# Kernel tuning notes

Hardware: AMD Instinct MI355X
Metric: run time of the kernel (lower is better)

The kernel has to match this reference:

```python
import jax, jax.numpy as jnp
import numpy as np

NUM_BOND_TYPE = 6
NUM_BOND_DIRECTION = 3
N_NODES = 20000
N_EDGES = 320000
HIDDEN = 256
OUT = 256
N_MASK = 2000


def setup_inputs() -> dict:
    key = jax.random.key(0)
    ks = jax.random.split(key, 12)
    x = jax.random.normal(ks[0], (N_NODES, HIDDEN), dtype=jnp.float32)
    edge_index = jax.random.randint(ks[1], (2, N_EDGES), 0, N_NODES, dtype=jnp.int64)
    edge_attr = jax.random.randint(ks[2], (N_EDGES, 2), 0, 3, dtype=jnp.int64)
    mask_node_indices = jax.random.randint(ks[3], (N_MASK,), 0, N_NODES, dtype=jnp.int64)
    # parameters (torch Linear convention: y = x @ W.T + b)
    def xavier(k, shape):
        fan_in, fan_out = shape[1], shape[0]
        lim = float(np.sqrt(6.0 / (fan_in + fan_out)))
        return jax.random.uniform(k, shape, jnp.float32, -lim, lim)
    prelu_a = jnp.asarray(0.25, dtype=jnp.float32)  # torch PReLU default
    W_enc = xavier(ks[4], (HIDDEN, HIDDEN))          # enc_to_dec, no bias
    E1 = xavier(ks[5], (NUM_BOND_TYPE, HIDDEN))
    E2 = xavier(ks[6], (NUM_BOND_DIRECTION, HIDDEN))
    W1 = xavier(ks[7], (2 * HIDDEN, HIDDEN))
    b1 = jnp.zeros((2 * HIDDEN,), jnp.float32)
    W2 = xavier(ks[8], (OUT, 2 * HIDDEN))
    b2 = jnp.zeros((OUT,), jnp.float32)
    return {"x": x, "edge_index": edge_index, "edge_attr": edge_attr,
            "mask_node_indices": mask_node_indices, "prelu_a": prelu_a,
            "W_enc": W_enc, "E1": E1, "E2": E2,
            "W1": W1, "b1": b1, "W2": W2, "b2": b2}


def reference(x, edge_index, edge_attr, mask_node_indices, prelu_a,
              W_enc, E1, E2, W1, b1, W2, b2):
    N = x.shape[0]
    # PReLU -> enc_to_dec linear (no bias) -> zero masked rows
    x = jnp.where(x >= 0, x, prelu_a * x)
    x = x @ W_enc.T
    x = x.at[mask_node_indices].set(0.0)
    # add self loops: (i,i) edges with attr (4, 0)
    loop = jnp.arange(N, dtype=edge_index.dtype)
    ei = jnp.concatenate([edge_index, jnp.stack([loop, loop])], axis=1)  # [2, E+N]
    loop_attr = jnp.concatenate(
        [jnp.full((N, 1), 4, edge_attr.dtype), jnp.zeros((N, 1), edge_attr.dtype)], axis=1)
    ea = jnp.concatenate([edge_attr, loop_attr], axis=0)                 # [E+N, 2]
    edge_emb = E1[ea[:, 0]] + E2[ea[:, 1]]                               # [E+N, D]
    src, dst = ei[0], ei[1]                                              # j -> i
    msg = x[src] + edge_emb                                              # [E+N, D]
    aggr = jax.ops.segment_sum(msg, dst, num_segments=N)                 # [N, D]
    # GIN MLP: Linear -> ReLU -> Linear
    h = jax.nn.relu(aggr @ W1.T + b1)
    return h @ W2.T + b2
```

## Files before the change

### kernel.cpp

```cpp
#include <hip/hip_runtime.h>

#define HIDDEN 256
#define CAP 64

typedef _Float16 h4_t __attribute__((ext_vector_type(4)));
typedef _Float16 h8_t __attribute__((ext_vector_type(8)));
typedef float    f4_t __attribute__((ext_vector_type(4)));

typedef const __attribute__((address_space(1))) void* gbl_ptr_t;
typedef __attribute__((address_space(3))) void*       lds_ptr_t;

__global__ __launch_bounds__(256) void k_prep(
        const float* __restrict__ x, _Float16* __restrict__ xh,
        const float* __restrict__ prelu_a, int M, int Mpad, int nb_x,
        const int* __restrict__ ei, const int* __restrict__ ea, int E,
        int* __restrict__ cnt, int* __restrict__ csr, int nb_fill,
        const float* __restrict__ W_enc, const float* __restrict__ W1,
        const float* __restrict__ W2, _Float16* __restrict__ Whenc,
        _Float16* __restrict__ Wh1, _Float16* __restrict__ Wh2, int nb_w,
        const int* __restrict__ mask, unsigned char* __restrict__ flags, int NM) {
    int b = blockIdx.x;
    int t = threadIdx.x;
    if (b < nb_x) {
        int base = (b * 256 + t) * 4;
        if (base >= Mpad * HIDDEN) return;
        int row = base >> 8;
        h4_t o;
        if (row < M) {
            float pa = *prelu_a;
            f4_t v = *(const f4_t*)(x + base);
            o.x = (_Float16)(v.x >= 0.f ? v.x : pa * v.x);
            o.y = (_Float16)(v.y >= 0.f ? v.y : pa * v.y);
            o.z = (_Float16)(v.z >= 0.f ? v.z : pa * v.z);
            o.w = (_Float16)(v.w >= 0.f ? v.w : pa * v.w);
        } else {
            o = (h4_t)(_Float16)0.f;
        }
        *(h4_t*)(xh + base) = o;
        return;
    }
    b -= nb_x;
    if (b < nb_fill) {
        int e = b * 256 + t;
        if (e >= E) return;
        int src = ei[e];
        int dst = ei[E + e];
        int combo = ea[2 * e] * 3 + ea[2 * e + 1];
        int slot = atomicAdd(&cnt[dst], 1);
        csr[dst * CAP + slot] = src | (combo << 16);
        return;
    }
    b -= nb_fill;
    if (b < nb_w) {
        const int n0 = HIDDEN * HIDDEN, n1 = 2 * HIDDEN * HIDDEN, n2 = HIDDEN * 2 * HIDDEN;
        int base = (b * 256 + t) * 4;
        const float* s; _Float16* d; int off;
        if (base < n0) { s = W_enc; d = Whenc; off = base; }
        else if (base < n0 + n1) { s = W1; d = Wh1; off = base - n0; }
        else if (base < n0 + n1 + n2) { s = W2; d = Wh2; off = base - n0 - n1; }
        else return;
        f4_t v = *(const f4_t*)(s + off);
        h4_t o; o.x = (_Float16)v.x; o.y = (_Float16)v.y;
        o.z = (_Float16)v.z; o.w = (_Float16)v.w;
        *(h4_t*)(d + off) = o;
        return;
    }
    b -= nb_w;
    {
        int i = b * 256 + t;
        if (i < NM) flags[mask[i]] = 1;
    }
}

__global__ __launch_bounds__(256) void k_aggregate(
        const _Float16* __restrict__ xe,
        const float* __restrict__ E1, const float* __restrict__ E2,
        const int* __restrict__ cnt, const int* __restrict__ csr,
        _Float16* __restrict__ aggr, int N, int Mpad) {
    __shared__ float e12[18 * HIDDEN];
    int t = threadIdx.x;
    for (int idx = t; idx < 18 * HIDDEN; idx += 256) {
        int combo = idx >> 8, c = idx & 255;
        int a1 = combo / 3, a2 = combo - a1 * 3;
        e12[idx] = E1[a1 * HIDDEN + c] + E2[a2 * HIDDEN + c];
    }
    __syncthreads();
    int node = blockIdx.x * 4 + (t >> 6);
    if (node >= Mpad) return;
    int lane = t & 63;
    int c0 = lane * 4;
    if (node >= N) {
        *(h4_t*)(aggr + (size_t)node * HIDDEN + c0) = (h4_t)(_Float16)0.f;
        return;
    }

    h4_t hs = *(const h4_t*)(xe + (size_t)node * HIDDEN + c0);
    const f4_t se = *(const f4_t*)&e12[12 * HIDDEN + c0];
    f4_t acc;
    acc.x = (float)hs.x + se.x; acc.y = (float)hs.y + se.y;
    acc.z = (float)hs.z + se.z; acc.w = (float)hs.w + se.w;

    const int* lst = csr + (size_t)node * CAP;
    int deg = cnt[node];
    int e = 0;
    for (; e + 1 < deg; e += 2) {
        int p0 = lst[e], p1 = lst[e + 1];
        h4_t h0 = *(const h4_t*)(xe + (size_t)(p0 & 0xFFFF) * HIDDEN + c0);
        h4_t h1 = *(const h4_t*)(xe + (size_t)(p1 & 0xFFFF) * HIDDEN + c0);
        f4_t e0 = *(const f4_t*)&e12[(p0 >> 16) * HIDDEN + c0];
        f4_t e1 = *(const f4_t*)&e12[(p1 >> 16) * HIDDEN + c0];
        acc.x += (float)h0.x + e0.x + (float)h1.x + e1.x;
        acc.y += (float)h0.y + e0.y + (float)h1.y + e1.y;
        acc.z += (float)h0.z + e0.z + (float)h1.z + e1.z;
        acc.w += (float)h0.w + e0.w + (float)h1.w + e1.w;
    }
    if (e < deg) {
        int p0 = lst[e];
        h4_t h0 = *(const h4_t*)(xe + (size_t)(p0 & 0xFFFF) * HIDDEN + c0);
        f4_t e0 = *(const f4_t*)&e12[(p0 >> 16) * HIDDEN + c0];
        acc.x += (float)h0.x + e0.x; acc.y += (float)h0.y + e0.y;
        acc.z += (float)h0.z + e0.z; acc.w += (float)h0.w + e0.w;
    }
    h4_t o;
    o.x = (_Float16)acc.x; o.y = (_Float16)acc.y;
    o.z = (_Float16)acc.z; o.w = (_Float16)acc.w;
    *(h4_t*)(aggr + (size_t)node * HIDDEN + c0) = o;
}

template <bool RELU, bool HAS_BIAS, bool OUT_F16, bool MASK>
__global__ __launch_bounds__(256) void k_mfma_gemm(
        const _Float16* __restrict__ A, const _Float16* __restrict__ B,
        const float* __restrict__ bias, void* __restrict__ Cout,
        const unsigned char* __restrict__ flags,
        int Mstore, int N, int K) {
    __shared__ _Float16 As[128 * 32];
    __shared__ _Float16 Bs[128 * 32];
    int t = threadIdx.x;
    int w = t >> 6, L = t & 63;
    int m0 = blockIdx.x * 128, n0 = blockIdx.y * 128;
    int wm = (w >> 1) * 64, wn = (w & 1) * 64;
    int lrow = L & 15, lk = (L >> 4) * 8;

    f4_t acc[4][4] = {};

    int c0 = t, c1 = t + 256;
    int r0 = c0 >> 2, o0 = (c0 & 3) * 8;
    int r1 = c1 >> 2, o1 = (c1 & 3) * 8;

    for (int k0 = 0; k0 < K; k0 += 32) {
        __builtin_amdgcn_global_load_lds((gbl_ptr_t)(A + (size_t)(m0 + r0) * K + k0 + o0),
                                         (lds_ptr_t)(As + c0 * 8), 16, 0, 0);
        __builtin_amdgcn_global_load_lds((gbl_ptr_t)(A + (size_t)(m0 + r1) * K + k0 + o1),
                                         (lds_ptr_t)(As + c1 * 8), 16, 0, 0);
        __builtin_amdgcn_global_load_lds((gbl_ptr_t)(B + (size_t)(n0 + r0) * K + k0 + o0),
                                         (lds_ptr_t)(Bs + c0 * 8), 16, 0, 0);
        __builtin_amdgcn_global_load_lds((gbl_ptr_t)(B + (size_t)(n0 + r1) * K + k0 + o1),
                                         (lds_ptr_t)(Bs + c1 * 8), 16, 0, 0);
        __syncthreads();

        h8_t af[4], bf[4];
#pragma unroll
        for (int i = 0; i < 4; ++i)
            af[i] = *(const h8_t*)&As[(wm + i * 16 + lrow) * 32 + lk];
#pragma unroll
        for (int j = 0; j < 4; ++j)
            bf[j] = *(const h8_t*)&Bs[(wn + j * 16 + lrow) * 32 + lk];
#pragma unroll
        for (int i = 0; i < 4; ++i)
#pragma unroll
            for (int j = 0; j < 4; ++j)
                acc[i][j] = __builtin_amdgcn_mfma_f32_16x16x32_f16(af[i], bf[j], acc[i][j], 0, 0, 0);
        __syncthreads();
    }

    int lcol = L & 15, lr4 = (L >> 4) * 4;
    float zmul[4][4];
#pragma unroll
    for (int i = 0; i < 4; ++i)
#pragma unroll
        for (int r = 0; r < 4; ++r) {
            int row = m0 + wm + i * 16 + lr4 + r;
            zmul[i][r] = (MASK && flags[row]) ? 0.f : 1.f;
        }
#pragma unroll
    for (int j = 0; j < 4; ++j) {
        int col = n0 + wn + j * 16 + lcol;
        float bv = HAS_BIAS ? bias[col] : 0.f;
#pragma unroll
        for (int i = 0; i < 4; ++i) {
#pragma unroll
            for (int r = 0; r < 4; ++r) {
                int row = m0 + wm + i * 16 + lr4 + r;
                float v = (acc[i][j][r] + bv) * zmul[i][r];
                if (RELU) v = v > 0.f ? v : 0.f;
                if (OUT_F16) {
                    ((_Float16*)Cout)[(size_t)row * N + col] = (_Float16)v;
                } else {
                    if (row < Mstore) ((float*)Cout)[(size_t)row * N + col] = v;
                }
            }
        }
    }
}

extern "C" void kernel_launch(void* const* d_in, const int* in_sizes, int n_in,
                              void* d_out, int out_size, void* d_ws, size_t ws_size,
                              hipStream_t stream) {
    const float* x       = (const float*)d_in[0];
    const int*   ei      = (const int*)d_in[1];
    const int*   ea      = (const int*)d_in[2];
    const int*   mask    = (const int*)d_in[3];
    const float* prelu_a = (const float*)d_in[4];
    const float* W_enc   = (const float*)d_in[5];
    const float* E1      = (const float*)d_in[6];
    const float* E2      = (const float*)d_in[7];
    const float* W1      = (const float*)d_in[8];
    const float* b1      = (const float*)d_in[9];
    const float* W2      = (const float*)d_in[10];
    const float* b2      = (const float*)d_in[11];
    float*       out     = (float*)d_out;

    int N  = in_sizes[0] / HIDDEN;
    int E  = in_sizes[1] / 2;
    int NM = in_sizes[3];
    int Mpad = ((N + 127) / 128) * 128;

    char* ws = (char*)d_ws;
    size_t off = 0;
    _Float16* xh    = (_Float16*)(ws + off); off += (size_t)Mpad * HIDDEN * 2;
    _Float16* XEh   = (_Float16*)(ws + off); off += (size_t)Mpad * HIDDEN * 2;
    _Float16* AGh   = (_Float16*)(ws + off); off += (size_t)Mpad * HIDDEN * 2;
    _Float16* Hh    = (_Float16*)(ws + off); off += (size_t)Mpad * 2 * HIDDEN * 2;
    _Float16* Whenc = (_Float16*)(ws + off); off += (size_t)HIDDEN * HIDDEN * 2;
    _Float16* Wh1   = (_Float16*)(ws + off); off += (size_t)2 * HIDDEN * HIDDEN * 2;
    _Float16* Wh2   = (_Float16*)(ws + off); off += (size_t)HIDDEN * 2 * HIDDEN * 2;
    int* cnt        = (int*)(ws + off);      off += (size_t)N * 4;
    unsigned char* flags = (unsigned char*)(ws + off); off += (size_t)Mpad;
    off = (off + 15) & ~(size_t)15;
    int* csr        = (int*)(ws + off);      off += (size_t)N * CAP * 4;

    hipMemsetAsync(cnt, 0, (size_t)N * 4 + (size_t)Mpad, stream);

    int nb_x    = (Mpad * HIDDEN / 4 + 255) / 256;
    int nb_fill = (E + 255) / 256;
    int wtot4   = (HIDDEN * HIDDEN + 2 * HIDDEN * HIDDEN + HIDDEN * 2 * HIDDEN) / 4;
    int nb_w    = (wtot4 + 255) / 256;
    int nb_m    = (NM + 255) / 256;
    k_prep<<<nb_x + nb_fill + nb_w + nb_m, 256, 0, stream>>>(
        x, xh, prelu_a, N, Mpad, nb_x,
        ei, ea, E, cnt, csr, nb_fill,
        W_enc, W1, W2, Whenc, Wh1, Wh2, nb_w,
        mask, flags, NM);

    dim3 g1(Mpad / 128, HIDDEN / 128);
    k_mfma_gemm<false, false, true, true><<<g1, 256, 0, stream>>>(
        xh, Whenc, nullptr, XEh, flags, N, HIDDEN, HIDDEN);

    k_aggregate<<<(Mpad + 3) / 4, 256, 0, stream>>>(XEh, E1, E2, cnt, csr, AGh, N, Mpad);

    dim3 g2(Mpad / 128, 2 * HIDDEN / 128);
    k_mfma_gemm<true, true, true, false><<<g2, 256, 0, stream>>>(
        AGh, Wh1, b1, Hh, nullptr, N, 2 * HIDDEN, HIDDEN);

    dim3 g3(Mpad / 128, HIDDEN / 128);
    k_mfma_gemm<false, true, false, false><<<g3, 256, 0, stream>>>(
        Hh, Wh2, b2, out, nullptr, N, HIDDEN, 2 * HIDDEN);
}
```

Baseline: 188.7 us.

## Double-buffer GEMM tiles, shrink to 128x64 blocks, and use fp16 adds in aggregation

The GEMM kernel now uses 2-wave 128-thread blocks with 128x64 output tiles and double-buffered LDS staging, so the next K slice loads while MFMAs run and one barrier per step is removed. The aggregation kernel stores the edge-embedding table as fp16, unrolls the neighbour loop by four, and sums pairs of messages in fp16 before accumulating in fp32. This aims to cut load latency stalls and LDS traffic, at the cost of some precision in the fp16 partial sums and a changed GEMM occupancy and tiling.

```diff
diff --git a/kernel.cpp b/kernel.cpp
--- a/kernel.cpp
+++ b/kernel.cpp
@@ -77,49 +77,60 @@
         const float* __restrict__ E1, const float* __restrict__ E2,
         const int* __restrict__ cnt, const int* __restrict__ csr,
         _Float16* __restrict__ aggr, int N, int Mpad) {
-    __shared__ float e12[18 * HIDDEN];
+    __shared__ __align__(16) _Float16 e12h[18 * HIDDEN];
     int t = threadIdx.x;
-    for (int idx = t; idx < 18 * HIDDEN; idx += 256) {
-        int combo = idx >> 8, c = idx & 255;
+    for (int idx = t; idx < 18 * 64; idx += 256) {
+        int combo = idx >> 6, c4 = (idx & 63) * 4;
         int a1 = combo / 3, a2 = combo - a1 * 3;
-        e12[idx] = E1[a1 * HIDDEN + c] + E2[a2 * HIDDEN + c];
+        f4_t v1 = *(const f4_t*)(E1 + a1 * HIDDEN + c4);
+        f4_t v2 = *(const f4_t*)(E2 + a2 * HIDDEN + c4);
+        h4_t o;
+        o.x = (_Float16)(v1.x + v2.x); o.y = (_Float16)(v1.y + v2.y);
+        o.z = (_Float16)(v1.z + v2.z); o.w = (_Float16)(v1.w + v2.w);
+        *(h4_t*)(e12h + combo * HIDDEN + c4) = o;
     }
     __syncthreads();
     int node = blockIdx.x * 4 + (t >> 6);
     if (node >= Mpad) return;
-    int lane = t & 63;
-    int c0 = lane * 4;
+    int c0 = (t & 63) * 4;
     if (node >= N) {
         *(h4_t*)(aggr + (size_t)node * HIDDEN + c0) = (h4_t)(_Float16)0.f;
         return;
     }
 
     h4_t hs = *(const h4_t*)(xe + (size_t)node * HIDDEN + c0);
-    const f4_t se = *(const f4_t*)&e12[12 * HIDDEN + c0];
+    h4_t se = *(const h4_t*)(e12h + 12 * HIDDEN + c0);
     f4_t acc;
-    acc.x = (float)hs.x + se.x; acc.y = (float)hs.y + se.y;
-    acc.z = (float)hs.z + se.z; acc.w = (float)hs.w + se.w;
+    acc.x = (float)hs.x + (float)se.x; acc.y = (float)hs.y + (float)se.y;
+    acc.z = (float)hs.z + (float)se.z; acc.w = (float)hs.w + (float)se.w;
 
     const int* lst = csr + (size_t)node * CAP;
     int deg = cnt[node];
     int e = 0;
-    for (; e + 1 < deg; e += 2) {
-        int p0 = lst[e], p1 = lst[e + 1];
+    for (; e + 3 < deg; e += 4) {
+        int p0 = lst[e], p1 = lst[e + 1], p2 = lst[e + 2], p3 = lst[e + 3];
         h4_t h0 = *(const h4_t*)(xe + (size_t)(p0 & 0xFFFF) * HIDDEN + c0);
         h4_t h1 = *(const h4_t*)(xe + (size_t)(p1 & 0xFFFF) * HIDDEN + c0);
-        f4_t e0 = *(const f4_t*)&e12[(p0 >> 16) * HIDDEN + c0];
-        f4_t e1 = *(const f4_t*)&e12[(p1 >> 16) * HIDDEN + c0];
-        acc.x += (float)h0.x + e0.x + (float)h1.x + e1.x;
-        acc.y += (float)h0.y + e0.y + (float)h1.y + e1.y;
-        acc.z += (float)h0.z + e0.z + (float)h1.z + e1.z;
-        acc.w += (float)h0.w + e0.w + (float)h1.w + e1.w;
-    }
-    if (e < deg) {
+        h4_t h2 = *(const h4_t*)(xe + (size_t)(p2 & 0xFFFF) * HIDDEN + c0);
+        h4_t h3 = *(const h4_t*)(xe + (size_t)(p3 & 0xFFFF) * HIDDEN + c0);
+        h4_t q0 = *(const h4_t*)(e12h + (p0 >> 16) * HIDDEN + c0);
+        h4_t q1 = *(const h4_t*)(e12h + (p1 >> 16) * HIDDEN + c0);
+        h4_t q2 = *(const h4_t*)(e12h + (p2 >> 16) * HIDDEN + c0);
+        h4_t q3 = *(const h4_t*)(e12h + (p3 >> 16) * HIDDEN + c0);
+        h4_t s01 = (h0 + q0) + (h1 + q1);
+        h4_t s23 = (h2 + q2) + (h3 + q3);
+        acc.x += (float)s01.x + (float)s23.x;
+        acc.y += (float)s01.y + (float)s23.y;
+        acc.z += (float)s01.z + (float)s23.z;
+        acc.w += (float)s01.w + (float)s23.w;
+    }
+    for (; e < deg; ++e) {
         int p0 = lst[e];
         h4_t h0 = *(const h4_t*)(xe + (size_t)(p0 & 0xFFFF) * HIDDEN + c0);
-        f4_t e0 = *(const f4_t*)&e12[(p0 >> 16) * HIDDEN + c0];
-        acc.x += (float)h0.x + e0.x; acc.y += (float)h0.y + e0.y;
-        acc.z += (float)h0.z + e0.z; acc.w += (float)h0.w + e0.w;
+        h4_t q0 = *(const h4_t*)(e12h + (p0 >> 16) * HIDDEN + c0);
+        h4_t s0 = h0 + q0;
+        acc.x += (float)s0.x; acc.y += (float)s0.y;
+        acc.z += (float)s0.z; acc.w += (float)s0.w;
     }
     h4_t o;
     o.x = (_Float16)acc.x; o.y = (_Float16)acc.y;
@@ -128,49 +139,56 @@
 }
 
 template <bool RELU, bool HAS_BIAS, bool OUT_F16, bool MASK>
-__global__ __launch_bounds__(256) void k_mfma_gemm(
+__global__ __launch_bounds__(128) void k_mfma_gemm(
         const _Float16* __restrict__ A, const _Float16* __restrict__ B,
         const float* __restrict__ bias, void* __restrict__ Cout,
         const unsigned char* __restrict__ flags,
         int Mstore, int N, int K) {
-    __shared__ _Float16 As[128 * 32];
-    __shared__ _Float16 Bs[128 * 32];
+    __shared__ __align__(16) _Float16 As[2][128 * 32];
+    __shared__ __align__(16) _Float16 Bs[2][64 * 32];
     int t = threadIdx.x;
     int w = t >> 6, L = t & 63;
-    int m0 = blockIdx.x * 128, n0 = blockIdx.y * 128;
-    int wm = (w >> 1) * 64, wn = (w & 1) * 64;
+    int m0 = blockIdx.x * 128, n0 = blockIdx.y * 64;
+    int wm = w * 64;
     int lrow = L & 15, lk = (L >> 4) * 8;
 
     f4_t acc[4][4] = {};
 
-    int c0 = t, c1 = t + 256;
-    int r0 = c0 >> 2, o0 = (c0 & 3) * 8;
-    int r1 = c1 >> 2, o1 = (c1 & 3) * 8;
-
-    for (int k0 = 0; k0 < K; k0 += 32) {
-        __builtin_amdgcn_global_load_lds((gbl_ptr_t)(A + (size_t)(m0 + r0) * K + k0 + o0),
-                                         (lds_ptr_t)(As + c0 * 8), 16, 0, 0);
-        __builtin_amdgcn_global_load_lds((gbl_ptr_t)(A + (size_t)(m0 + r1) * K + k0 + o1),
-                                         (lds_ptr_t)(As + c1 * 8), 16, 0, 0);
-        __builtin_amdgcn_global_load_lds((gbl_ptr_t)(B + (size_t)(n0 + r0) * K + k0 + o0),
-                                         (lds_ptr_t)(Bs + c0 * 8), 16, 0, 0);
-        __builtin_amdgcn_global_load_lds((gbl_ptr_t)(B + (size_t)(n0 + r1) * K + k0 + o1),
-                                         (lds_ptr_t)(Bs + c1 * 8), 16, 0, 0);
+    auto stage = [&](int k0, int b) {
+#pragma unroll
+        for (int i = 0; i < 4; ++i) {
+            int c = t + 128 * i;
+            __builtin_amdgcn_global_load_lds(
+                (gbl_ptr_t)(A + (size_t)(m0 + (c >> 2)) * K + k0 + (c & 3) * 8),
+                (lds_ptr_t)(&As[b][c * 8]), 16, 0, 0);
+        }
+#pragma unroll
+        for (int i = 0; i < 2; ++i) {
+            int c = t + 128 * i;
+            __builtin_amdgcn_global_load_lds(
+                (gbl_ptr_t)(B + (size_t)(n0 + (c >> 2)) * K + k0 + (c & 3) * 8),
+                (lds_ptr_t)(&Bs[b][c * 8]), 16, 0, 0);
+        }
+    };
+
+    stage(0, 0);
+    int nstep = K >> 5;
+    for (int s = 0; s < nstep; ++s) {
+        int b = s & 1;
         __syncthreads();
-
+        if (s + 1 < nstep) stage((s + 1) << 5, b ^ 1);
         h8_t af[4], bf[4];
 #pragma unroll
         for (int i = 0; i < 4; ++i)
-            af[i] = *(const h8_t*)&As[(wm + i * 16 + lrow) * 32 + lk];
+            af[i] = *(const h8_t*)&As[b][(wm + i * 16 + lrow) * 32 + lk];
 #pragma unroll
         for (int j = 0; j < 4; ++j)
-            bf[j] = *(const h8_t*)&Bs[(wn + j * 16 + lrow) * 32 + lk];
+            bf[j] = *(const h8_t*)&Bs[b][(j * 16 + lrow) * 32 + lk];
 #pragma unroll
         for (int i = 0; i < 4; ++i)
 #pragma unroll
             for (int j = 0; j < 4; ++j)
                 acc[i][j] = __builtin_amdgcn_mfma_f32_16x16x32_f16(af[i], bf[j], acc[i][j], 0, 0, 0);
-        __syncthreads();
     }
 
     int lcol = L & 15, lr4 = (L >> 4) * 4;
@@ -184,7 +202,7 @@
         }
 #pragma unroll
     for (int j = 0; j < 4; ++j) {
-        int col = n0 + wn + j * 16 + lcol;
+        int col = n0 + j * 16 + lcol;
         float bv = HAS_BIAS ? bias[col] : 0.f;
 #pragma unroll
         for (int i = 0; i < 4; ++i) {
@@ -252,17 +270,17 @@
         W_enc, W1, W2, Whenc, Wh1, Wh2, nb_w,
         mask, flags, NM);
 
-    dim3 g1(Mpad / 128, HIDDEN / 128);
-    k_mfma_gemm<false, false, true, true><<<g1, 256, 0, stream>>>(
+    dim3 g1(Mpad / 128, HIDDEN / 64);
+    k_mfma_gemm<false, false, true, true><<<g1, 128, 0, stream>>>(
         xh, Whenc, nullptr, XEh, flags, N, HIDDEN, HIDDEN);
 
     k_aggregate<<<(Mpad + 3) / 4, 256, 0, stream>>>(XEh, E1, E2, cnt, csr, AGh, N, Mpad);
 
-    dim3 g2(Mpad / 128, 2 * HIDDEN / 128);
-    k_mfma_gemm<true, true, true, false><<<g2, 256, 0, stream>>>(
+    dim3 g2(Mpad / 128, 2 * HIDDEN / 64);
+    k_mfma_gemm<true, true, true, false><<<g2, 128, 0, stream>>>(
         AGh, Wh1, b1, Hh, nullptr, N, 2 * HIDDEN, HIDDEN);
 
-    dim3 g3(Mpad / 128, HIDDEN / 128);
-    k_mfma_gemm<false, true, false, false><<<g3, 256, 0, stream>>>(
+    dim3 g3(Mpad / 128, HIDDEN / 64);
+    k_mfma_gemm<false, true, false, false><<<g3, 128, 0, stream>>>(
         Hh, Wh2, b2, out, nullptr, N, HIDDEN, 2 * HIDDEN);
 }
```

Result: slower. 194.9 us (+3.3%).
